# Kernel optimization log

Measured on AMD Instinct MI355X. Metric: run time of the kernel, lower is better.

Reference implementation:

```python
import jax, jax.numpy as jnp
import numpy as np

N_DR, N_P, N_DIS = 8000, 20000, 5000
N_MF, N_BP, N_CC, N_PATH = 3000, 8000, 2000, 2392
H, B = 128, 65536
F_FINGER, F_SEQ, F_DIS = 1024, 400, 512
EPS = 1e-5


def _gcn(e, xs, ndst, W, b):
    # DGL GraphConv(norm='none', in==out): sum-aggregate src feats, then linear, then ReLU
    agg = jax.ops.segment_sum(xs[e[0]], e[1], num_segments=ndst)
    return jax.nn.relu(agg @ W + b)


def _sage(e, xs, xd, Wp, bp, Ws, Wn, b):
    # DGL SAGEConv(aggregator_type='pool'): max over relu(fc_pool(src)) + fc_self(dst), then ReLU
    h = jax.nn.relu(xs @ Wp + bp)
    agg = jax.ops.segment_max(h[e[0]], e[1], num_segments=xd.shape[0])
    agg = jnp.where(jnp.isfinite(agg), agg, 0.0)  # zero-in-degree dst -> 0 (DGL convention)
    return jax.nn.relu(xd @ Ws + agg @ Wn + b)


def _bn_relu(x, g, b):
    # BatchNorm1d in training mode (batch stats, biased var) + ReLU
    m = x.mean(0)
    v = x.var(0)
    return jax.nn.relu(g * (x - m) * jax.lax.rsqrt(v + EPS) + b)


def setup_inputs():
    key = jax.random.key(0)
    ks = iter(jax.random.split(key, 80))
    def nrm(shape, s=0.05):
        return jax.random.normal(next(ks), shape, dtype=jnp.float32) * s
    def edges(E, ns, nd):
        k1, k2 = jax.random.split(next(ks))
        return jnp.stack([jax.random.randint(k1, (E,), 0, ns, dtype=jnp.int32),
                          jax.random.randint(k2, (E,), 0, nd, dtype=jnp.int32)])
    inp = {}
    inp["x_dr"] = jax.random.randint(next(ks), (B, 1), 0, N_DR, dtype=jnp.int32)
    inp["x_p"] = jax.random.randint(next(ks), (B, 1), 0, N_P, dtype=jnp.int32)
    inp["finger_feats"] = nrm((N_DR, F_FINGER), 1.0)
    inp["seq_feats"] = nrm((N_P, F_SEQ), 1.0)
    inp["disease_feat"] = nrm((N_DIS, F_DIS), 1.0)
    inp["MF_feat"] = jnp.eye(N_MF, dtype=jnp.float32)   # identity feats, as in source
    inp["BP_feat"] = jnp.eye(N_BP, dtype=jnp.float32)
    inp["CC_feat"] = jnp.eye(N_CC, dtype=jnp.float32)
    inp["Pathway_feat"] = jnp.eye(N_PATH, dtype=jnp.float32)
    inp["e_dtdr"] = edges(100000, N_DIS, N_DR)
    inp["e_dmdr"] = edges(100000, N_DIS, N_DR)
    inp["e_dp"] = edges(200000, N_DIS, N_P)
    inp["e_drtd"] = edges(100000, N_DR, N_DIS)
    inp["e_drmd"] = edges(100000, N_DR, N_DIS)
    inp["e_pd"] = edges(200000, N_P, N_DIS)
    inp["e_ddi"] = edges(300000, N_DR, N_DR)
    inp["e_ppi"] = edges(600000, N_P, N_P)
    inp["e_mf_sim"] = edges(100000, N_MF, N_MF)
    inp["e_bp_sim"] = edges(300000, N_BP, N_BP)
    inp["e_cc_sim"] = edges(60000, N_CC, N_CC)
    inp["e_mf2p"] = edges(200000, N_MF, N_P)
    inp["e_bp2p"] = edges(400000, N_BP, N_P)
    inp["e_cc2p"] = edges(100000, N_CC, N_P)
    inp["e_path2p"] = edges(100000, N_PATH, N_P)
    inp["W_dr_emb"] = nrm((F_FINGER, H)); inp["b_dr_emb"] = jnp.zeros((H,), jnp.float32)
    inp["W_p_emb"] = nrm((F_SEQ, H)); inp["b_p_emb"] = jnp.zeros((H,), jnp.float32)
    inp["W_d_emb"] = nrm((F_DIS, H)); inp["b_d_emb"] = jnp.zeros((H,), jnp.float32)
    inp["W_mf_emb"] = nrm((N_MF, H)); inp["b_mf_emb"] = jnp.zeros((H,), jnp.float32)
    inp["W_bp_emb"] = nrm((N_BP, H)); inp["b_bp_emb"] = jnp.zeros((H,), jnp.float32)
    inp["W_cc_emb"] = nrm((N_CC, H)); inp["b_cc_emb"] = jnp.zeros((H,), jnp.float32)
    inp["W_path_emb"] = nrm((N_PATH, H)); inp["b_path_emb"] = jnp.zeros((H,), jnp.float32)
    inp["W_gcn"] = nrm((7, H, H)); inp["b_gcn"] = jnp.zeros((7, H), jnp.float32)
    inp["Wp_sage"] = nrm((8, H, H)); inp["bp_sage"] = jnp.zeros((8, H), jnp.float32)
    inp["Ws_sage"] = nrm((8, H, H)); inp["Wn_sage"] = nrm((8, H, H))
    inp["b_sage"] = jnp.zeros((8, H), jnp.float32)
    inp["W1"] = nrm((7 * H, 2 * H)); inp["b1"] = jnp.zeros((2 * H,), jnp.float32)
    inp["g1"] = jnp.ones((2 * H,), jnp.float32); inp["be1"] = jnp.zeros((2 * H,), jnp.float32)
    inp["W2"] = nrm((2 * H, H)); inp["b2"] = jnp.zeros((H,), jnp.float32)
    inp["g2"] = jnp.ones((H,), jnp.float32); inp["be2"] = jnp.zeros((H,), jnp.float32)
    inp["W3"] = nrm((H, 64)); inp["b3"] = jnp.zeros((64,), jnp.float32)
    inp["g3"] = jnp.ones((64,), jnp.float32); inp["be3"] = jnp.zeros((64,), jnp.float32)
    inp["Wo"] = nrm((64, 1)); inp["bo"] = jnp.zeros((1,), jnp.float32)
    return inp


def reference(x_dr, x_p, e_dtdr, e_dmdr, e_dp, e_drtd, e_drmd, e_pd, e_ddi, e_ppi,
              e_mf_sim, e_bp_sim, e_cc_sim, e_mf2p, e_bp2p, e_cc2p, e_path2p,
              finger_feats, seq_feats, disease_feat, MF_feat, BP_feat, CC_feat, Pathway_feat,
              W_dr_emb, b_dr_emb, W_p_emb, b_p_emb, W_d_emb, b_d_emb,
              W_mf_emb, b_mf_emb, W_bp_emb, b_bp_emb, W_cc_emb, b_cc_emb, W_path_emb, b_path_emb,
              W_gcn, b_gcn, Wp_sage, bp_sage, Ws_sage, Wn_sage, b_sage,
              W1, b1, g1, be1, W2, b2, g2, be2, W3, b3, g3, be3, Wo, bo):
    relu = jax.nn.relu
    # node-type input embeddings (Linear + ReLU)
    h_dr0 = relu(finger_feats @ W_dr_emb + b_dr_emb)
    h_p0 = relu(seq_feats @ W_p_emb + b_p_emb)
    h_d = relu(disease_feat @ W_d_emb + b_d_emb)
    h_mf = relu(MF_feat @ W_mf_emb + b_mf_emb)
    h_bp = relu(BP_feat @ W_bp_emb + b_bp_emb)
    h_cc = relu(CC_feat @ W_cc_emb + b_cc_emb)
    h_path = relu(Pathway_feat @ W_path_emb + b_path_emb)
    # GO similarity GCNs with residual
    mf = _gcn(e_mf_sim, h_mf, N_MF, W_gcn[0], b_gcn[0]) + h_mf
    bp = _gcn(e_bp_sim, h_bp, N_BP, W_gcn[1], b_gcn[1]) + h_bp
    cc = _gcn(e_cc_sim, h_cc, N_CC, W_gcn[2], b_gcn[2]) + h_cc
    # GO->protein and pathway->protein (HeteroGraphConv, sum aggregate)
    h_p_go = (_gcn(e_mf2p, mf, N_P, W_gcn[3], b_gcn[3])
              + _gcn(e_bp2p, bp, N_P, W_gcn[4], b_gcn[4])
              + _gcn(e_cc2p, cc, N_P, W_gcn[5], b_gcn[5]))
    h_p_path = _gcn(e_path2p, h_path, N_P, W_gcn[6], b_gcn[6])
    # heterogeneous SAGE layer over my_G (weights shared across the two applications)
    def S(i):
        return (Wp_sage[i], bp_sage[i], Ws_sage[i], Wn_sage[i], b_sage[i])
    def hetero(hdr, hp, hd):
        dr = (_sage(e_dtdr, hd, hdr, *S(0)) + _sage(e_dmdr, hd, hdr, *S(1))
              + _sage(e_ddi, hdr, hdr, *S(6)))
        p = _sage(e_dp, hd, hp, *S(2)) + _sage(e_ppi, hp, hp, *S(7))
        d = (_sage(e_drtd, hdr, hd, *S(3)) + _sage(e_drmd, hdr, hd, *S(4))
             + _sage(e_pd, hp, hd, *S(5)))
        return dr, p, d
    dr1, p1, d1 = hetero(h_dr0, h_p0, h_d)
    dr2, p2, _ = hetero(dr1, p1, d1)
    dr_new = jnp.concatenate([h_dr0, dr1, dr2], axis=1)                 # [N_DR, 3H]
    p_new = jnp.concatenate([h_p0, p1, p2, h_p_go + h_p_path], axis=1)  # [N_P, 4H]
    h = jnp.concatenate([dr_new[x_dr[:, 0]], p_new[x_p[:, 0]]], axis=1)  # [B, 7H]
    h = _bn_relu(h @ W1 + b1, g1, be1)
    h = _bn_relu(h @ W2 + b2, g2, be2)
    h = _bn_relu(h @ W3 + b3, g3, be3)
    return jax.nn.sigmoid(h @ Wo + bo)
```

## Files before the change

kernel.cpp:

```cpp
#include <hip/hip_runtime.h>

#define NCSR 15
#define MAXP 6
#define MAXT 8
#define MAXG 12
#define NPT 21
#define NWT 37

typedef __attribute__((ext_vector_type(8))) short bfrag;
typedef __attribute__((ext_vector_type(4))) float ffrag;

__device__ __forceinline__ float b2f(unsigned short s) {
  return __uint_as_float(((unsigned int)s) << 16);
}
__device__ __forceinline__ unsigned short f2b(float f) {
  unsigned int u = __float_as_uint(f);
  u = (u + 0x7FFFu + ((u >> 16) & 1u)) >> 16;
  return (unsigned short)u;
}
__device__ __forceinline__ float ldf(const void* p, size_t i, int bf) {
  if (bf) return b2f(((const unsigned short*)p)[i]);
  return ((const float*)p)[i];
}
__device__ __forceinline__ int4 ld8(const void* p, size_t i, int bf) {
  if (bf) return *(const int4*)((const unsigned short*)p + i);
  const float* pf = (const float*)p + i;
  float4 f0 = *(const float4*)pf;
  float4 f1 = *(const float4*)(pf + 4);
  int4 v;
  v.x = (int)((unsigned)f2b(f0.x) | ((unsigned)f2b(f0.y) << 16));
  v.y = (int)((unsigned)f2b(f0.z) | ((unsigned)f2b(f0.w) << 16));
  v.z = (int)((unsigned)f2b(f1.x) | ((unsigned)f2b(f1.y) << 16));
  v.w = (int)((unsigned)f2b(f1.z) | ((unsigned)f2b(f1.w) << 16));
  return v;
}

struct CsrDesc {
  const int* src; const int* dst; int E; int n_dst;
  int* rowptr; unsigned short* csrc; int* slot; int pad;
};
struct CsrArgs { CsrDesc d[NCSR]; };

struct PTask { const void* src; float* dst; int n; int pad; };
struct PArgs { PTask t[NPT]; };

struct WTask { const void* src; unsigned short* dst; int K; int N; int eoff; int pad; };
struct WArgs { WTask t[NWT]; };

struct MPass { const unsigned short* A; const unsigned short* W; const float* bias; int lda; int ldw; int flags; };
struct MTask {
  MPass p[MAXP];
  const unsigned short* R; unsigned short* C;
  int npass, n, K, ldc, relu, pad;
};

struct GTask { const int* rowptr; const unsigned short* csrc; const unsigned short* X; unsigned short* out; int n_dst; int ldx; int mode; int pad; };

struct ETask { const void* A; const unsigned short* W; const float* bias; unsigned short* C; int n, K, ldc, pad; };
struct EArgs { ETask t[3]; };

struct BTask { const void* w; const float* b; unsigned short* out; int n; int pad[3]; };
struct BArgs { BTask t[4]; };

struct GSup { GTask t[MAXG]; int off[MAXG + 1]; int nt; };
struct MSup { MTask t[MAXT]; int off[MAXT + 1]; int nt; };

__device__ __forceinline__ int find_task(const int* off, int nt, int bx, int& lx) {
  int t = 0;
  while (t + 1 < nt && bx >= off[t + 1]) ++t;
  lx = bx - off[t];
  return t;
}


__device__ void count_body(const CsrDesc& cd, int lx) {
  for (int e = lx * 256 + (int)threadIdx.x; e < cd.E; e += 96 * 256)
    cd.slot[e] = atomicAdd(&cd.rowptr[cd.dst[e] + 1], 1);
}

__device__ void fill_body(const CsrDesc& cd, int lx) {
  for (int e = lx * 256 + (int)threadIdx.x; e < cd.E; e += 96 * 256) {
    int d = cd.dst[e];
    cd.csrc[cd.rowptr[d] + cd.slot[e]] = (unsigned short)cd.src[e];
  }
}

__device__ void bias_body(const BTask& T, int lx, int bf) {
  const int n8 = T.n >> 3;
  for (int i = lx * 256 + (int)threadIdx.x; i < n8; i += 128 * 256) {
    int base = i << 3;
    int4 v = ld8(T.w, (size_t)base, bf);
    const unsigned short* pv = (const unsigned short*)&v;
    const int cb = base & 127;
    unsigned short o[8];
#pragma unroll
    for (int j = 0; j < 8; ++j) {
      float f = b2f(pv[j]) + T.b[cb + j];
      o[j] = f2b(f > 0.f ? f : 0.f);
    }
    *(int4*)(T.out + base) = *(const int4*)o;
  }
}

__device__ void gather_body(const GTask& T, int lx) {
  int w = lx * 4 + ((int)threadIdx.x >> 6);
  if (w >= T.n_dst) return;
  int lane = threadIdx.x & 63;
  int beg = T.rowptr[w], end = T.rowptr[w + 1];
  float a0 = 0.f, a1 = 0.f;
  int j = beg;
  if (T.mode == 0) {
    for (; j + 3 < end; j += 4) {
      unsigned int u0 = ((const unsigned int*)(T.X + (size_t)T.csrc[j] * T.ldx))[lane];
      unsigned int u1 = ((const unsigned int*)(T.X + (size_t)T.csrc[j + 1] * T.ldx))[lane];
      unsigned int u2 = ((const unsigned int*)(T.X + (size_t)T.csrc[j + 2] * T.ldx))[lane];
      unsigned int u3 = ((const unsigned int*)(T.X + (size_t)T.csrc[j + 3] * T.ldx))[lane];
      a0 += __uint_as_float(u0 << 16) + __uint_as_float(u1 << 16)
          + __uint_as_float(u2 << 16) + __uint_as_float(u3 << 16);
      a1 += __uint_as_float(u0 & 0xFFFF0000u) + __uint_as_float(u1 & 0xFFFF0000u)
          + __uint_as_float(u2 & 0xFFFF0000u) + __uint_as_float(u3 & 0xFFFF0000u);
    }
    for (; j < end; ++j) {
      unsigned int u0 = ((const unsigned int*)(T.X + (size_t)T.csrc[j] * T.ldx))[lane];
      a0 += __uint_as_float(u0 << 16);
      a1 += __uint_as_float(u0 & 0xFFFF0000u);
    }
  } else {
    for (; j + 3 < end; j += 4) {
      unsigned int u0 = ((const unsigned int*)(T.X + (size_t)T.csrc[j] * T.ldx))[lane];
      unsigned int u1 = ((const unsigned int*)(T.X + (size_t)T.csrc[j + 1] * T.ldx))[lane];
      unsigned int u2 = ((const unsigned int*)(T.X + (size_t)T.csrc[j + 2] * T.ldx))[lane];
      unsigned int u3 = ((const unsigned int*)(T.X + (size_t)T.csrc[j + 3] * T.ldx))[lane];
      a0 = fmaxf(fmaxf(a0, fmaxf(__uint_as_float(u0 << 16), __uint_as_float(u1 << 16))),
                 fmaxf(__uint_as_float(u2 << 16), __uint_as_float(u3 << 16)));
      a1 = fmaxf(fmaxf(a1, fmaxf(__uint_as_float(u0 & 0xFFFF0000u), __uint_as_float(u1 & 0xFFFF0000u))),
                 fmaxf(__uint_as_float(u2 & 0xFFFF0000u), __uint_as_float(u3 & 0xFFFF0000u)));
    }
    for (; j < end; ++j) {
      unsigned int u0 = ((const unsigned int*)(T.X + (size_t)T.csrc[j] * T.ldx))[lane];
      a0 = fmaxf(a0, __uint_as_float(u0 << 16));
      a1 = fmaxf(a1, __uint_as_float(u0 & 0xFFFF0000u));
    }
  }
  unsigned int* po = (unsigned int*)(T.out + (size_t)w * 128);
  po[lane] = (unsigned int)f2b(a0) | ((unsigned int)f2b(a1) << 16);
}

__device__ void mg_body(const MTask* T, int lx) {
  const int n = T->n;
  const int row0 = lx * 64;
  if (row0 >= n) return;
  __shared__ __align__(16) unsigned short As[64][72];
  __shared__ __align__(16) unsigned short Ws[128][72];
  const int t = threadIdx.x;
  const int wave = t >> 6, lane = t & 63;
  const int m16 = lane & 15, kq = lane >> 4;
  const int K = T->K;
  ffrag acc[4][2], accO[4][2];
#pragma unroll
  for (int i = 0; i < 4; ++i)
#pragma unroll
    for (int j = 0; j < 2; ++j) { acc[i][j] = (ffrag)0.f; accO[i][j] = (ffrag)0.f; }
  const int colbase = wave * 32;
  for (int ip = 0; ip < T->npass; ++ip) {
    const unsigned short* Ap = T->p[ip].A;
    const unsigned short* Wp = T->p[ip].W;
    const int lda = T->p[ip].lda, ldw = T->p[ip].ldw;
    for (int k0 = 0; k0 < K; k0 += 64) {
      __syncthreads();
#pragma unroll
      for (int e = t; e < 512; e += 256) {
        int r = e >> 3, c = e & 7;
        int row = row0 + r;
        int4 v = {0, 0, 0, 0};
        if (row < n) v = *(const int4*)(Ap + (size_t)row * lda + k0 + c * 8);
        *(int4*)&As[r][c * 8] = v;
      }
#pragma unroll
      for (int e = t; e < 1024; e += 256) {
        int nn = e >> 3, c = e & 7;
        *(int4*)&Ws[nn][c * 8] = *(const int4*)(Wp + (size_t)nn * ldw + k0 + c * 8);
      }
      __syncthreads();
#pragma unroll
      for (int kk = 0; kk < 64; kk += 32) {
        bfrag b0 = *(const bfrag*)&Ws[colbase + m16][kk + kq * 8];
        bfrag b1 = *(const bfrag*)&Ws[colbase + 16 + m16][kk + kq * 8];
#pragma unroll
        for (int rb = 0; rb < 4; ++rb) {
          bfrag a = *(const bfrag*)&As[rb * 16 + m16][kk + kq * 8];
          acc[rb][0] = __builtin_amdgcn_mfma_f32_16x16x32_bf16(a, b0, acc[rb][0], 0, 0, 0);
          acc[rb][1] = __builtin_amdgcn_mfma_f32_16x16x32_bf16(a, b1, acc[rb][1], 0, 0, 0);
        }
      }
    }
    if (T->p[ip].flags & 1) {
      const float* bias = T->p[ip].bias;
      float bv0 = bias ? bias[colbase + m16] : 0.f;
      float bv1 = bias ? bias[colbase + 16 + m16] : 0.f;
#pragma unroll
      for (int rb = 0; rb < 4; ++rb)
#pragma unroll
        for (int cb = 0; cb < 2; ++cb) {
          float bv = cb ? bv1 : bv0;
#pragma unroll
          for (int r = 0; r < 4; ++r) {
            float v = acc[rb][cb][r] + bv;
            if (T->relu) v = v > 0.f ? v : 0.f;
            accO[rb][cb][r] += v;
          }
          acc[rb][cb] = (ffrag)0.f;
        }
    }
  }
  const int ldc = T->ldc;
#pragma unroll
  for (int rb = 0; rb < 4; ++rb)
#pragma unroll
    for (int cb = 0; cb < 2; ++cb) {
      int col = colbase + cb * 16 + m16;
#pragma unroll
      for (int r = 0; r < 4; ++r) {
        int row = row0 + rb * 16 + kq * 4 + r;
        if (row < n) {
          float v = accO[rb][cb][r];
          if (T->R) v += b2f(T->R[(size_t)row * ldc + col]);
          T->C[(size_t)row * ldc + col] = f2b(v);
        }
      }
    }
}

__device__ void embed_body(const ETask& T, int lx, int bf) {
  const int n = T.n;
  const int row0 = lx * 32;
  if (row0 >= n) return;
  __shared__ __align__(16) unsigned short As[32][72];
  __shared__ __align__(16) unsigned short Ws[128][72];
  const int t = threadIdx.x;
  const int wave = t >> 6, lane = t & 63;
  const int m16 = lane & 15, kq = lane >> 4;
  const int K = T.K;
  ffrag acc[2][2];
#pragma unroll
  for (int i = 0; i < 2; ++i)
#pragma unroll
    for (int j = 0; j < 2; ++j) acc[i][j] = (ffrag)0.f;
  const int colbase = wave * 32;
  for (int k0 = 0; k0 < K; k0 += 64) {
    __syncthreads();
    {
      int r = t >> 3, c = t & 7;
      int row = row0 + r, k = k0 + c * 8;
      int4 v = {0, 0, 0, 0};
      if (row < n && k < K) v = ld8(T.A, (size_t)row * K + k, bf);
      *(int4*)&As[r][c * 8] = v;
    }
#pragma unroll
    for (int e = t; e < 1024; e += 256) {
      int nn = e >> 3, c = e & 7;
      int4 v = {0, 0, 0, 0};
      if (k0 + c * 8 < K) v = *(const int4*)(T.W + (size_t)nn * K + k0 + c * 8);
      *(int4*)&Ws[nn][c * 8] = v;
    }
    __syncthreads();
#pragma unroll
    for (int kk = 0; kk < 64; kk += 32) {
      bfrag a0 = *(const bfrag*)&As[m16][kk + kq * 8];
      bfrag a1 = *(const bfrag*)&As[16 + m16][kk + kq * 8];
      bfrag b0 = *(const bfrag*)&Ws[colbase + m16][kk + kq * 8];
      bfrag b1 = *(const bfrag*)&Ws[colbase + 16 + m16][kk + kq * 8];
      acc[0][0] = __builtin_amdgcn_mfma_f32_16x16x32_bf16(a0, b0, acc[0][0], 0, 0, 0);
      acc[0][1] = __builtin_amdgcn_mfma_f32_16x16x32_bf16(a0, b1, acc[0][1], 0, 0, 0);
      acc[1][0] = __builtin_amdgcn_mfma_f32_16x16x32_bf16(a1, b0, acc[1][0], 0, 0, 0);
      acc[1][1] = __builtin_amdgcn_mfma_f32_16x16x32_bf16(a1, b1, acc[1][1], 0, 0, 0);
    }
  }
#pragma unroll
  for (int rb = 0; rb < 2; ++rb)
#pragma unroll
    for (int cb = 0; cb < 2; ++cb) {
      int col = colbase + cb * 16 + m16;
      float bv = T.bias[col];
#pragma unroll
      for (int r = 0; r < 4; ++r) {
        int row = row0 + rb * 16 + kq * 4 + r;
        if (row < n) {
          float v = acc[rb][cb][r] + bv;
          T.C[(size_t)row * T.ldc + col] = f2b(v > 0.f ? v : 0.f);
        }
      }
    }
}


__global__ void k_flag(const unsigned int* probe, int* flag) {
  if (threadIdx.x == 0) *flag = (probe[0] == 0x3F800000u) ? 0 : 1;
}

__launch_bounds__(256)
__global__ void k_cv(PArgs pa, WArgs wa, const int* __restrict__ flagp) {
  const int bf = *flagp;
  int bx = blockIdx.x;
  if (bx < NPT * 4) {
    const PTask T = pa.t[bx >> 2];
    for (int i = (bx & 3) * 256 + (int)threadIdx.x; i < T.n; i += 4 * 256)
      T.dst[i] = ldf(T.src, (size_t)i, bf);
  } else {
    bx -= NPT * 4;
    const WTask T = wa.t[bx >> 5];
    const int lx = bx & 31;
    const int total = T.K * T.N;
    const size_t eoff = (size_t)T.eoff;
    for (int i = lx * 256 + (int)threadIdx.x; i < total; i += 32 * 256) {
      int n = i / T.K, k = i - n * T.K;
      T.dst[i] = f2b(ldf(T.src, eoff + (size_t)k * T.N + n, bf));
    }
  }
}

__launch_bounds__(256)
__global__ void k_prep(CsrArgs csr, EArgs ea, BArgs ba, const int* __restrict__ flagp) {
  int bx = blockIdx.x;
  if (bx < NCSR * 96) { count_body(csr.d[bx / 96], bx % 96); return; }
  bx -= NCSR * 96;
  if (bx < 1032) {
    int t, lx;
    if (bx < 250) { t = 0; lx = bx; }
    else if (bx < 875) { t = 1; lx = bx - 250; }
    else { t = 2; lx = bx - 875; }
    embed_body(ea.t[t], lx, *flagp);
    return;
  }
  bx -= 1032;
  bias_body(ba.t[bx >> 7], bx & 127, *flagp);
}

__global__ void k_csr_scan(CsrArgs args) {
  const CsrDesc cd = args.d[blockIdx.x];
  const int n = cd.n_dst + 1;
  const int t = threadIdx.x;
  const int lane = t & 63, w = t >> 6;
  __shared__ int wsum[16];
  int carry = 0;
  for (int base = 0; base < n; base += 1024) {
    int i = base + t;
    int v = (i < n) ? cd.rowptr[i] : 0;
    for (int off = 1; off < 64; off <<= 1) {
      int u = __shfl_up(v, off, 64);
      if (lane >= off) v += u;
    }
    if (lane == 63) wsum[w] = v;
    __syncthreads();
    if (w == 0) {
      int s = (lane < 16) ? wsum[lane] : 0;
      for (int off = 1; off < 16; off <<= 1) {
        int u = __shfl_up(s, off, 64);
        if (lane >= off) s += u;
      }
      if (lane < 16) wsum[lane] = s;
    }
    __syncthreads();
    int nv = v + carry + (w > 0 ? wsum[w - 1] : 0);
    if (i < n) cd.rowptr[i] = nv;
    carry += wsum[15];
    __syncthreads();
  }
}

__launch_bounds__(256)
__global__ void k_fillmg(CsrArgs csr, MSup ms) {
  int bx = blockIdx.x;
  if (bx < NCSR * 96) { fill_body(csr.d[bx / 96], bx % 96); return; }
  bx -= NCSR * 96;
  int lx; int t = find_task(ms.off, ms.nt, bx, lx);
  mg_body(&ms.t[t], lx);
}

__global__ void k_gsup(GSup gs) {
  int lx; int t = find_task(gs.off, gs.nt, blockIdx.x, lx);
  gather_body(gs.t[t], lx);
}

__launch_bounds__(256)
__global__ void k_gm(GSup gs, MSup ms) {
  int bx = blockIdx.x;
  const int gtot = gs.off[gs.nt];
  if (bx < gtot) {
    int lx; int t = find_task(gs.off, gs.nt, bx, lx);
    gather_body(gs.t[t], lx);
    return;
  }
  bx -= gtot;
  int lx; int t = find_task(ms.off, ms.nt, bx, lx);
  mg_body(&ms.t[t], lx);
}

template<int NC>
__launch_bounds__(256)
__global__ void k_gemm_bn(const unsigned short* __restrict__ A, const unsigned short* __restrict__ W,
                          const float* __restrict__ bias, const float* __restrict__ ss,
                          unsigned short* __restrict__ C, double* __restrict__ st, int n, int K) {
  constexpr int CB = NC / 64;
  __shared__ __align__(16) unsigned short As[64][72];
  __shared__ __align__(16) unsigned short Ws[NC][72];
  const int t = threadIdx.x;
  const int wave = t >> 6, lane = t & 63;
  const int m16 = lane & 15, kq = lane >> 4;
  const int row0 = blockIdx.x * 64;
  if (row0 >= n) return;
  ffrag acc[4][CB];
#pragma unroll
  for (int i = 0; i < 4; ++i)
#pragma unroll
    for (int j = 0; j < CB; ++j) acc[i][j] = (ffrag)0.f;
  const int colbase = wave * 16 * CB;
  for (int k0 = 0; k0 < K; k0 += 64) {
    __syncthreads();
#pragma unroll
    for (int e = t; e < 512; e += 256) {
      int r = e >> 3, c = e & 7;
      int row = row0 + r, k = k0 + c * 8;
      int4 v = {0, 0, 0, 0};
      if (row < n) {
        int4 a8 = *(const int4*)(A + (size_t)row * K + k);
        const unsigned short* pa = (const unsigned short*)&a8;
        unsigned short o[8];
#pragma unroll
        for (int j = 0; j < 8; ++j) {
          float val = fmaf(b2f(pa[j]), ss[k + j], ss[K + k + j]);
          o[j] = f2b(val > 0.f ? val : 0.f);
        }
        v = *(const int4*)o;
      }
      *(int4*)&As[r][c * 8] = v;
    }
#pragma unroll
    for (int e = t; e < NC * 8; e += 256) {
      int nn = e >> 3, c = e & 7;
      *(int4*)&Ws[nn][c * 8] = *(const int4*)(W + (size_t)nn * K + k0 + c * 8);
    }
    __syncthreads();
#pragma unroll
    for (int kk = 0; kk < 64; kk += 32) {
#pragma unroll
      for (int cb = 0; cb < CB; ++cb) {
        bfrag b = *(const bfrag*)&Ws[colbase + cb * 16 + m16][kk + kq * 8];
#pragma unroll
        for (int rb = 0; rb < 4; ++rb) {
          bfrag a = *(const bfrag*)&As[rb * 16 + m16][kk + kq * 8];
          acc[rb][cb] = __builtin_amdgcn_mfma_f32_16x16x32_bf16(a, b, acc[rb][cb], 0, 0, 0);
        }
      }
    }
  }
#pragma unroll
  for (int cb = 0; cb < CB; ++cb) {
    int col = colbase + cb * 16 + m16;
    float bv = bias[col];
    float cs = 0.f, cq = 0.f;
#pragma unroll
    for (int rb = 0; rb < 4; ++rb) {
#pragma unroll
      for (int r = 0; r < 4; ++r) {
        int row = row0 + rb * 16 + kq * 4 + r;
        if (row < n) {
          float v = acc[rb][cb][r] + bv;
          C[(size_t)row * NC + col] = f2b(v);
          cs += v; cq += v * v;
        }
      }
    }
    cs += __shfl_xor(cs, 16); cs += __shfl_xor(cs, 32);
    cq += __shfl_xor(cq, 16); cq += __shfl_xor(cq, 32);
    if (kq == 0) {
      atomicAdd(&st[col], (double)cs);
      atomicAdd(&st[NC + col], (double)cq);
    }
  }
}

__global__ void k_hstat(const int* __restrict__ xdr, const int* __restrict__ xp,
                        const unsigned short* __restrict__ Udr, const unsigned short* __restrict__ Up,
                        double* __restrict__ st, int B) {
  __shared__ double sS[4][256];
  __shared__ double sQ[4][256];
  const int t = threadIdx.x;
  const int lane = t & 63, w = t >> 6;
  const int c4 = lane * 4;
  double s0 = 0, s1 = 0, s2 = 0, s3 = 0, q0 = 0, q1 = 0, q2 = 0, q3 = 0;
  const int NW = gridDim.x * 4;
  for (int r = blockIdx.x * 4 + w; r < B; r += NW) {
    int i = xdr[r], j = xp[r];
    uint2 a = *(const uint2*)(Udr + (size_t)i * 256 + c4);
    uint2 b = *(const uint2*)(Up + (size_t)j * 256 + c4);
    float v0 = b2f((unsigned short)a.x) + b2f((unsigned short)b.x);
    float v1 = b2f((unsigned short)(a.x >> 16)) + b2f((unsigned short)(b.x >> 16));
    float v2 = b2f((unsigned short)a.y) + b2f((unsigned short)b.y);
    float v3 = b2f((unsigned short)(a.y >> 16)) + b2f((unsigned short)(b.y >> 16));
    s0 += v0; s1 += v1; s2 += v2; s3 += v3;
    q0 += (double)v0 * (double)v0; q1 += (double)v1 * (double)v1;
    q2 += (double)v2 * (double)v2; q3 += (double)v3 * (double)v3;
  }
  sS[w][c4] = s0; sS[w][c4 + 1] = s1; sS[w][c4 + 2] = s2; sS[w][c4 + 3] = s3;
  sQ[w][c4] = q0; sQ[w][c4 + 1] = q1; sQ[w][c4 + 2] = q2; sQ[w][c4 + 3] = q3;
  __syncthreads();
  double ts = sS[0][t] + sS[1][t] + sS[2][t] + sS[3][t];
  double tq = sQ[0][t] + sQ[1][t] + sQ[2][t] + sQ[3][t];
  atomicAdd(&st[t], ts);
  atomicAdd(&st[256 + t], tq);
}

__launch_bounds__(256)
__global__ void k_gemm_bn1(const int* __restrict__ xdr, const int* __restrict__ xp,
                           const unsigned short* __restrict__ Udr, const unsigned short* __restrict__ Up,
                           const unsigned short* __restrict__ W, const float* __restrict__ bias,
                           const float* __restrict__ ss, unsigned short* __restrict__ Co,
                           double* __restrict__ st, int n) {
  __shared__ __align__(16) unsigned short As[64][72];
  __shared__ __align__(16) unsigned short Ws[128][72];
  __shared__ int gi[64], gj[64];
  const int t = threadIdx.x;
  const int wave = t >> 6, lane = t & 63;
  const int m16 = lane & 15, kq = lane >> 4;
  const int row0 = blockIdx.x * 64;
  if (row0 >= n) return;
  if (t < 64) {
    int row = row0 + t; if (row >= n) row = n - 1;
    gi[t] = xdr[row]; gj[t] = xp[row];
  }
  ffrag acc[4][2];
#pragma unroll
  for (int i = 0; i < 4; ++i)
#pragma unroll
    for (int j = 0; j < 2; ++j) acc[i][j] = (ffrag)0.f;
  const int colbase = wave * 32;
  __syncthreads();
  for (int k0 = 0; k0 < 256; k0 += 64) {
    __syncthreads();
#pragma unroll
    for (int e = t; e < 512; e += 256) {
      int r = e >> 3, seg = e & 7;
      int k = k0 + seg * 8;
      int4 a = *(const int4*)(Udr + (size_t)gi[r] * 256 + k);
      int4 b = *(const int4*)(Up + (size_t)gj[r] * 256 + k);
      const unsigned short* pa = (const unsigned short*)&a;
      const unsigned short* pb = (const unsigned short*)&b;
      unsigned short o[8];
#pragma unroll
      for (int jj = 0; jj < 8; ++jj) {
        float v = b2f(pa[jj]) + b2f(pb[jj]);
        v = fmaf(v, ss[k + jj], ss[256 + k + jj]);
        o[jj] = f2b(v > 0.f ? v : 0.f);
      }
      *(int4*)&As[r][seg * 8] = *(const int4*)o;
    }
#pragma unroll
    for (int e = t; e < 1024; e += 256) {
      int nn = e >> 3, c = e & 7;
      *(int4*)&Ws[nn][c * 8] = *(const int4*)(W + (size_t)nn * 256 + k0 + c * 8);
    }
    __syncthreads();
#pragma unroll
    for (int kk = 0; kk < 64; kk += 32) {
      bfrag b0 = *(const bfrag*)&Ws[colbase + m16][kk + kq * 8];
      bfrag b1 = *(const bfrag*)&Ws[colbase + 16 + m16][kk + kq * 8];
#pragma unroll
      for (int rb = 0; rb < 4; ++rb) {
        bfrag a = *(const bfrag*)&As[rb * 16 + m16][kk + kq * 8];
        acc[rb][0] = __builtin_amdgcn_mfma_f32_16x16x32_bf16(a, b0, acc[rb][0], 0, 0, 0);
        acc[rb][1] = __builtin_amdgcn_mfma_f32_16x16x32_bf16(a, b1, acc[rb][1], 0, 0, 0);
      }
    }
  }
#pragma unroll
  for (int cb = 0; cb < 2; ++cb) {
    int col = colbase + cb * 16 + m16;
    float bv = bias[col];
    float cs = 0.f, cq = 0.f;
#pragma unroll
    for (int rb = 0; rb < 4; ++rb) {
#pragma unroll
      for (int r = 0; r < 4; ++r) {
        int row = row0 + rb * 16 + kq * 4 + r;
        if (row < n) {
          float v = acc[rb][cb][r] + bv;
          Co[(size_t)row * 128 + col] = f2b(v);
          cs += v; cq += v * v;
        }
      }
    }
    cs += __shfl_xor(cs, 16); cs += __shfl_xor(cs, 32);
    cq += __shfl_xor(cq, 16); cq += __shfl_xor(cq, 32);
    if (kq == 0) {
      atomicAdd(&st[col], (double)cs);
      atomicAdd(&st[128 + col], (double)cq);
    }
  }
}

__global__ void k_bnfin(const double* __restrict__ st, int B, int C,
                        const float* __restrict__ g, const float* __restrict__ be,
                        float* __restrict__ ss) {
  int c = threadIdx.x;
  if (c < C) {
    double m = st[c] / B;
    double v = st[C + c] / B - m * m;
    if (v < 0) v = 0;
    float sc = (float)((double)g[c] / sqrt(v + 1e-5));
    ss[c] = sc;
    ss[C + c] = be[c] - (float)m * sc;
  }
}

__global__ void k_final(const unsigned short* __restrict__ Z3, const float* __restrict__ ss3,
                        const float* __restrict__ Wo, const float* __restrict__ bo,
                        void* __restrict__ out, int B, const int* __restrict__ flagp) {
  __shared__ float w[64], sc[64], sh[64];
  if (threadIdx.x < 64) {
    w[threadIdx.x] = Wo[threadIdx.x];
    sc[threadIdx.x] = ss3[threadIdx.x];
    sh[threadIdx.x] = ss3[64 + threadIdx.x];
  }
  __syncthreads();
  const int bf = *flagp;
  const float bb = bo[0];
  for (int r = blockIdx.x * blockDim.x + threadIdx.x; r < B; r += gridDim.x * blockDim.x) {
    const unsigned short* z = &Z3[(size_t)r * 64];
    float acc = bb;
#pragma unroll
    for (int k = 0; k < 64; ++k) {
      float y = fmaf(b2f(z[k]), sc[k], sh[k]);
      y = y > 0.f ? y : 0.f;
      acc = fmaf(y, w[k], acc);
    }
    float sv = 1.f / (1.f + expf(-acc));
    if (bf) ((unsigned short*)out)[r] = f2b(sv);
    else ((float*)out)[r] = sv;
  }
}

extern "C" void kernel_launch(void* const* d_in, const int* in_sizes, int n_in,
                              void* d_out, int out_size, void* d_ws, size_t ws_size,
                              hipStream_t stream) {
  enum { N_DR = 8000, N_P = 20000, N_DIS = 5000, N_MF = 3000, N_BP = 8000,
         N_CC = 2000, N_PATH = 2392 };
  if (n_in < 59) return;
  const int B = in_sizes[0];
  const int* x_dr = (const int*)d_in[0];
  const int* x_p  = (const int*)d_in[1];

  char* base = (char*)d_ws;
  size_t off = 0;
  auto alloc = [&](size_t bytes) -> void* {
    void* p = base + off;
    off += (bytes + 255) & ~(size_t)255;
    return p;
  };
  int*    flagp = (int*)alloc(256);
  double* st1 = (double*)alloc(896 * sizeof(double));
  double* st2 = st1 + 512; double* st3 = st2 + 256;
  float*  ss1 = (float*)alloc(896 * sizeof(float));
  float*  ss2 = ss1 + 512; float* ss3 = ss2 + 256;
  float*  pbuf = (float*)alloc(6000 * sizeof(float));
  unsigned short* wbf = (unsigned short*)alloc(1100000 * 2);
  unsigned short* DR  = (unsigned short*)alloc((size_t)N_DR * 384 * 2);
  unsigned short* P   = (unsigned short*)alloc((size_t)N_P * 512 * 2);
  unsigned short* h_d = (unsigned short*)alloc((size_t)N_DIS * 128 * 2);
  unsigned short* d1b = (unsigned short*)alloc((size_t)N_DIS * 128 * 2);
  unsigned short* z1  = (unsigned short*)alloc((size_t)B * 256 * 2);
  char* arena = (char*)alloc(44u * 1024 * 1024);
  if (off > ws_size) return;

  unsigned short* ar = (unsigned short*)arena;
  unsigned short* A_hmf  = ar;
  unsigned short* A_hbp  = A_hmf + (size_t)N_MF * 128;
  unsigned short* A_hcc  = A_hbp + (size_t)N_BP * 128;
  unsigned short* A_hpath= A_hcc + (size_t)N_CC * 128;
  unsigned short* A_gomf = A_hpath + (size_t)N_PATH * 128;
  unsigned short* A_gobp = A_gomf + (size_t)N_MF * 128;
  unsigned short* A_gocc = A_gobp + (size_t)N_BP * 128;
  unsigned short* ag17 = A_gocc + (size_t)N_CC * 128;
  unsigned short* ag18 = ag17 + (size_t)N_MF * 128;
  unsigned short* ag9  = ag18 + (size_t)N_BP * 128;
  unsigned short* ag10 = ag9  + (size_t)N_DR * 128;
  unsigned short* ag11 = ag10 + (size_t)N_DR * 128;
  unsigned short* ag12 = ag11 + (size_t)N_P * 128;
  unsigned short* ag13 = ag12 + (size_t)N_DIS * 128;
  unsigned short* ag14 = ag13 + (size_t)N_DIS * 128;
  unsigned short* ag15 = ag14 + (size_t)N_DIS * 128;
  unsigned short* ag16 = ag15 + (size_t)N_DR * 128;
  unsigned short* ag21 = ag16 + (size_t)N_P * 128;
  unsigned short* ag22 = ag21 + (size_t)N_P * 128;
  unsigned short* ag23 = ag22 + (size_t)N_P * 128;
  unsigned short* U_dr = ar;
  unsigned short* U_p  = U_dr + (size_t)N_DR * 256;
  unsigned short* z2 = U_p + (size_t)N_P * 256;
  unsigned short* z3 = z1;
  int* slot_arena = (int*)(ar + (size_t)7168000);

  k_flag<<<1, 64, 0, stream>>>((const unsigned int*)d_in[5], flagp);

  float* pp[59] = {};
  PArgs pa;
  {
    const int pidx[NPT] = {25,27,29,31,33,35,37,39,41,44,46,47,48,50,51,52,54,55,56,57,58};
    size_t poff = 0;
    for (int l = 0; l < NPT; ++l) {
      int i = pidx[l];
      pa.t[l].src = d_in[i]; pa.t[l].dst = pbuf + poff; pa.t[l].n = in_sizes[i]; pa.t[l].pad = 0;
      pp[i] = pbuf + poff;
      poff += in_sizes[i];
    }
  }
  unsigned short *Wdr_t, *Wpe_t, *Wde_t, *Wg_t, *Wps_t, *Wss_t, *Wns_t, *W1_t, *W2_t, *W3_t;
  WArgs wa;
  {
    int l = 0; size_t woff = 0;
    auto add = [&](int inIdx, int eoff, int K, int N) -> unsigned short* {
      unsigned short* dst = wbf + woff;
      wa.t[l].src = d_in[inIdx]; wa.t[l].dst = dst; wa.t[l].K = K; wa.t[l].N = N;
      wa.t[l].eoff = eoff; wa.t[l].pad = 0;
      ++l; woff += (size_t)K * N;
      return dst;
    };
    Wdr_t = add(24, 0, 1024, 128);
    Wpe_t = add(26, 0, 400, 128);
    Wde_t = add(28, 0, 512, 128);
    Wg_t = wbf + woff;
    for (int j = 0; j < 7; ++j) add(38, j * 16384, 128, 128);
    Wps_t = wbf + woff;
    for (int j = 0; j < 8; ++j) add(40, j * 16384, 128, 128);
    Wss_t = wbf + woff;
    for (int j = 0; j < 8; ++j) add(42, j * 16384, 128, 128);
    Wns_t = wbf + woff;
    for (int j = 0; j < 8; ++j) add(43, j * 16384, 128, 128);
    W1_t = add(45, 0, 896, 256);
    W2_t = add(49, 0, 256, 128);
    W3_t = add(53, 0, 128, 64);
  }
  k_cv<<<NPT * 4 + NWT * 32, 256, 0, stream>>>(pa, wa, flagp);

  const int list_ei[NCSR] = {9, 10, 11, 12, 13, 14, 15, 16, 17, 18, 19, 20, 21, 22, 23};
  const int list_nd[NCSR] = {N_DR, N_DR, N_P, N_DIS, N_DIS, N_DIS, N_DR, N_P,
                             N_MF, N_BP, N_CC, N_P, N_P, N_P, N_P};
  int* rp[24]; unsigned short* cs[24];
  CsrArgs csra;
  unsigned short* csr_end;
  {
    int* ip = (int*)z1;
    int* rp0 = ip;
    for (int l = 0; l < NCSR; ++l) { csra.d[l].rowptr = ip; rp[list_ei[l]] = ip; ip += list_nd[l] + 1; }
    size_t rp_total = (size_t)(ip - rp0);
    unsigned short* up = (unsigned short*)ip;
    size_t slotoff = 0;
    for (int l = 0; l < NCSR; ++l) {
      int ei = list_ei[l];
      int E = in_sizes[ei] / 2;
      csra.d[l].src = (const int*)d_in[ei];
      csra.d[l].dst = (const int*)d_in[ei] + E;
      csra.d[l].E = E;
      csra.d[l].n_dst = list_nd[l];
      csra.d[l].csrc = up; cs[ei] = up;
      csra.d[l].slot = slot_arena + slotoff;
      csra.d[l].pad = 0;
      up += E;
      slotoff += E;
    }
    csr_end = up;
    hipMemsetAsync(rp0, 0, rp_total * sizeof(int), stream);
  }
  unsigned short* plb = (unsigned short*)(((uintptr_t)csr_end + 255) & ~(uintptr_t)255);
  unsigned short* plz0 = plb;
  unsigned short* plz1 = plz0 + (size_t)N_DIS * 128;
  unsigned short* plz2 = plz1 + (size_t)N_DIS * 128;
  unsigned short* plz3 = plz2 + (size_t)N_DIS * 128;
  unsigned short* plz4 = plz3 + (size_t)N_DR * 128;
  unsigned short* plz5 = plz4 + (size_t)N_DR * 128;
  unsigned short* plz6 = plz5 + (size_t)N_P * 128;
  unsigned short* plz7 = plz6 + (size_t)N_DR * 128;
  unsigned short* ag19 = plz7 + (size_t)N_P * 128;
  unsigned short* ag20 = ag19 + (size_t)N_CC * 128;
  if ((ag20 + (size_t)N_P * 128) > (z1 + (size_t)B * 256)) return;

  hipMemsetAsync(st1, 0, 896 * sizeof(double), stream);

  auto mkpass = [](MTask& T, int i, const unsigned short* A, int lda, const unsigned short* W,
                   int ldw, const float* bias, int end) {
    T.p[i].A = A; T.p[i].lda = lda; T.p[i].W = W; T.p[i].ldw = ldw;
    T.p[i].bias = bias; T.p[i].flags = end;
  };
  const float* bg = pp[39];
  const float* bp_s = pp[41];
  const float* b_s = pp[44];

  auto gadd = [](GSup& g, GTask t) {
    if (g.nt == 0) g.off[0] = 0;
    g.t[g.nt] = t;
    g.off[g.nt + 1] = g.off[g.nt] + (t.n_dst + 3) / 4;
    g.nt++;
  };
  auto madd = [](MSup& m, const MTask& t) {
    if (m.nt == 0) m.off[0] = 0;
    m.t[m.nt] = t;
    m.off[m.nt + 1] = m.off[m.nt] + (t.n + 63) / 64;
    m.nt++;
  };

  {
    EArgs ea;
    ea.t[0] = {d_in[2], Wdr_t, pp[25], DR, N_DR, 1024, 384, 0};
    ea.t[1] = {d_in[3], Wpe_t, pp[27], P, N_P, 400, 512, 0};
    ea.t[2] = {d_in[4], Wde_t, pp[29], h_d, N_DIS, 512, 128, 0};
    BArgs ba;
    ba.t[0] = {d_in[30], pp[31], A_hmf, N_MF * 128, {}};
    ba.t[1] = {d_in[32], pp[33], A_hbp, N_BP * 128, {}};
    ba.t[2] = {d_in[34], pp[35], A_hcc, N_CC * 128, {}};
    ba.t[3] = {d_in[36], pp[37], A_hpath, N_PATH * 128, {}};
    k_prep<<<NCSR * 96 + 1032 + 4 * 128, 256, 0, stream>>>(csra, ea, ba, flagp);
  }

  k_csr_scan<<<NCSR, 1024, 0, stream>>>(csra);

  {
    MSup ms; ms.nt = 0;
    const unsigned short* xs[8] = {h_d, h_d, h_d, DR, DR, P, DR, P};
    const int lda[8] = {128, 128, 128, 384, 384, 512, 384, 512};
    const int nn[8] = {N_DIS, N_DIS, N_DIS, N_DR, N_DR, N_P, N_DR, N_P};
    unsigned short* plo[8] = {plz0, plz1, plz2, plz3, plz4, plz5, plz6, plz7};
    for (int i = 0; i < 8; ++i) {
      MTask T;
      mkpass(T, 0, xs[i], lda[i], Wps_t + (size_t)i * 16384, 128, bp_s + i * 128, 1);
      T.npass = 1; T.n = nn[i]; T.K = 128; T.R = nullptr; T.C = plo[i]; T.ldc = 128; T.relu = 1;
      madd(ms, T);
    }
    k_fillmg<<<NCSR * 96 + ms.off[ms.nt], 256, 0, stream>>>(csra, ms);
  }

  {
    GSup gs; gs.nt = 0;
    gadd(gs, {rp[17], cs[17], A_hmf, ag17, N_MF, 128, 0, 0});
    gadd(gs, {rp[18], cs[18], A_hbp, ag18, N_BP, 128, 0, 0});
    gadd(gs, {rp[19], cs[19], A_hcc, ag19, N_CC, 128, 0, 0});
    gadd(gs, {rp[9],  cs[9],  plz0, ag9,  N_DR, 128, 1, 0});
    gadd(gs, {rp[10], cs[10], plz1, ag10, N_DR, 128, 1, 0});
    gadd(gs, {rp[11], cs[11], plz2, ag11, N_P, 128, 1, 0});
    gadd(gs, {rp[12], cs[12], plz3, ag12, N_DIS, 128, 1, 0});
    gadd(gs, {rp[13], cs[13], plz4, ag13, N_DIS, 128, 1, 0});
    gadd(gs, {rp[14], cs[14], plz5, ag14, N_DIS, 128, 1, 0});
    gadd(gs, {rp[15], cs[15], plz6, ag15, N_DR, 128, 1, 0});
    gadd(gs, {rp[16], cs[16], plz7, ag16, N_P, 128, 1, 0});
    k_gsup<<<gs.off[gs.nt], 256, 0, stream>>>(gs);
  }

  GSup g0; g0.nt = 0; g0.off[0] = 0;

  {
    MSup ms; ms.nt = 0;
    for (int i = 0; i < 3; ++i) {
      MTask T;
      const unsigned short* aggp = (i == 0) ? ag17 : (i == 1) ? ag18 : ag19;
      const unsigned short* Rp = (i == 0) ? A_hmf : (i == 1) ? A_hbp : A_hcc;
      unsigned short* Cp = (i == 0) ? A_gomf : (i == 1) ? A_gobp : A_gocc;
      int n = (i == 0) ? N_MF : (i == 1) ? N_BP : N_CC;
      mkpass(T, 0, aggp, 128, Wg_t + (size_t)i * 16384, 128, bg + i * 128, 1);
      T.npass = 1; T.n = n; T.K = 128; T.R = Rp; T.C = Cp; T.ldc = 128; T.relu = 1;
      madd(ms, T);
    }
    {
      MTask T;
      mkpass(T, 0, DR, 384, Wss_t + (size_t)0 * 16384, 128, nullptr, 0);
      mkpass(T, 1, ag9, 128, Wns_t + (size_t)0 * 16384, 128, b_s + 0 * 128, 1);
      mkpass(T, 2, DR, 384, Wss_t + (size_t)1 * 16384, 128, nullptr, 0);
      mkpass(T, 3, ag10, 128, Wns_t + (size_t)1 * 16384, 128, b_s + 1 * 128, 1);
      mkpass(T, 4, DR, 384, Wss_t + (size_t)6 * 16384, 128, nullptr, 0);
      mkpass(T, 5, ag15, 128, Wns_t + (size_t)6 * 16384, 128, b_s + 6 * 128, 1);
      T.npass = 6; T.n = N_DR; T.K = 128; T.R = nullptr; T.C = DR + 128; T.ldc = 384; T.relu = 1;
      madd(ms, T);
    }
    {
      MTask T;
      mkpass(T, 0, P, 512, Wss_t + (size_t)2 * 16384, 128, nullptr, 0);
      mkpass(T, 1, ag11, 128, Wns_t + (size_t)2 * 16384, 128, b_s + 2 * 128, 1);
      mkpass(T, 2, P, 512, Wss_t + (size_t)7 * 16384, 128, nullptr, 0);
      mkpass(T, 3, ag16, 128, Wns_t + (size_t)7 * 16384, 128, b_s + 7 * 128, 1);
      T.npass = 4; T.n = N_P; T.K = 128; T.R = nullptr; T.C = P + 128; T.ldc = 512; T.relu = 1;
      madd(ms, T);
    }
    {
      MTask T;
      mkpass(T, 0, h_d, 128, Wss_t + (size_t)3 * 16384, 128, nullptr, 0);
      mkpass(T, 1, ag12, 128, Wns_t + (size_t)3 * 16384, 128, b_s + 3 * 128, 1);
      mkpass(T, 2, h_d, 128, Wss_t + (size_t)4 * 16384, 128, nullptr, 0);
      mkpass(T, 3, ag13, 128, Wns_t + (size_t)4 * 16384, 128, b_s + 4 * 128, 1);
      mkpass(T, 4, h_d, 128, Wss_t + (size_t)5 * 16384, 128, nullptr, 0);
      mkpass(T, 5, ag14, 128, Wns_t + (size_t)5 * 16384, 128, b_s + 5 * 128, 1);
      T.npass = 6; T.n = N_DIS; T.K = 128; T.R = nullptr; T.C = d1b; T.ldc = 128; T.relu = 1;
      madd(ms, T);
    }
    k_gm<<<ms.off[ms.nt], 256, 0, stream>>>(g0, ms);
  }

  {
    GSup gs; gs.nt = 0;
    gadd(gs, {rp[20], cs[20], A_gomf, ag20, N_P, 128, 0, 0});
    gadd(gs, {rp[21], cs[21], A_gobp, ag21, N_P, 128, 0, 0});
    gadd(gs, {rp[22], cs[22], A_gocc, ag22, N_P, 128, 0, 0});
    gadd(gs, {rp[23], cs[23], A_hpath, ag23, N_P, 128, 0, 0});
    MSup ms; ms.nt = 0;
    const unsigned short* xs[5] = {d1b, d1b, d1b, DR + 128, P + 128};
    const int lda[5] = {128, 128, 128, 384, 512};
    const int nn[5] = {N_DIS, N_DIS, N_DIS, N_DR, N_P};
    unsigned short* plo[5] = {plz0, plz1, plz2, plz6, plz7};
    const int si[5] = {0, 1, 2, 6, 7};
    for (int i = 0; i < 5; ++i) {
      MTask T;
      mkpass(T, 0, xs[i], lda[i], Wps_t + (size_t)si[i] * 16384, 128, bp_s + si[i] * 128, 1);
      T.npass = 1; T.n = nn[i]; T.K = 128; T.R = nullptr; T.C = plo[i]; T.ldc = 128; T.relu = 1;
      madd(ms, T);
    }
    k_gm<<<gs.off[gs.nt] + ms.off[ms.nt], 256, 0, stream>>>(gs, ms);
  }

  {
    GSup gs; gs.nt = 0;
    gadd(gs, {rp[9],  cs[9],  plz0, ag9,  N_DR, 128, 1, 0});
    gadd(gs, {rp[10], cs[10], plz1, ag10, N_DR, 128, 1, 0});
    gadd(gs, {rp[11], cs[11], plz2, ag11, N_P, 128, 1, 0});
    gadd(gs, {rp[15], cs[15], plz6, ag15, N_DR, 128, 1, 0});
    gadd(gs, {rp[16], cs[16], plz7, ag16, N_P, 128, 1, 0});
    MSup ms; ms.nt = 0;
    MTask T;
    mkpass(T, 0, ag20, 128, Wg_t + 3 * 16384, 128, bg + 3 * 128, 1);
    mkpass(T, 1, ag21, 128, Wg_t + 4 * 16384, 128, bg + 4 * 128, 1);
    mkpass(T, 2, ag22, 128, Wg_t + 5 * 16384, 128, bg + 5 * 128, 1);
    mkpass(T, 3, ag23, 128, Wg_t + 6 * 16384, 128, bg + 6 * 128, 1);
    T.npass = 4; T.n = N_P; T.K = 128; T.R = nullptr; T.C = P + 384; T.ldc = 512; T.relu = 1;
    madd(ms, T);
    k_gm<<<gs.off[gs.nt] + ms.off[ms.nt], 256, 0, stream>>>(gs, ms);
  }

  {
    MSup ms; ms.nt = 0;
    {
      MTask T;
      mkpass(T, 0, DR + 128, 384, Wss_t + (size_t)0 * 16384, 128, nullptr, 0);
      mkpass(T, 1, ag9, 128, Wns_t + (size_t)0 * 16384, 128, b_s + 0 * 128, 1);
      mkpass(T, 2, DR + 128, 384, Wss_t + (size_t)1 * 16384, 128, nullptr, 0);
      mkpass(T, 3, ag10, 128, Wns_t + (size_t)1 * 16384, 128, b_s + 1 * 128, 1);
      mkpass(T, 4, DR + 128, 384, Wss_t + (size_t)6 * 16384, 128, nullptr, 0);
      mkpass(T, 5, ag15, 128, Wns_t + (size_t)6 * 16384, 128, b_s + 6 * 128, 1);
      T.npass = 6; T.n = N_DR; T.K = 128; T.R = nullptr; T.C = DR + 256; T.ldc = 384; T.relu = 1;
      madd(ms, T);
    }
    {
      MTask T;
      mkpass(T, 0, P + 128, 512, Wss_t + (size_t)2 * 16384, 128, nullptr, 0);
      mkpass(T, 1, ag11, 128, Wns_t + (size_t)2 * 16384, 128, b_s + 2 * 128, 1);
      mkpass(T, 2, P + 128, 512, Wss_t + (size_t)7 * 16384, 128, nullptr, 0);
      mkpass(T, 3, ag16, 128, Wns_t + (size_t)7 * 16384, 128, b_s + 7 * 128, 1);
      T.npass = 4; T.n = N_P; T.K = 128; T.R = nullptr; T.C = P + 256; T.ldc = 512; T.relu = 1;
      madd(ms, T);
    }
    k_gm<<<ms.off[ms.nt], 256, 0, stream>>>(g0, ms);
  }

  {
    MSup ms; ms.nt = 0;
    for (int half = 0; half < 2; ++half) {
      {
        MTask T;
        mkpass(T, 0, DR, 384, W1_t + (size_t)(half * 128) * 896, 896, pp[46] + half * 128, 1);
        T.npass = 1; T.n = N_DR; T.K = 384; T.R = nullptr;
        T.C = U_dr + half * 128; T.ldc = 256; T.relu = 0;
        madd(ms, T);
      }
      {
        MTask T;
        mkpass(T, 0, P, 512, W1_t + (size_t)(half * 128) * 896 + 384, 896, nullptr, 1);
        T.npass = 1; T.n = N_P; T.K = 512; T.R = nullptr;
        T.C = U_p + half * 128; T.ldc = 256; T.relu = 0;
        madd(ms, T);
      }
    }
    k_gm<<<ms.off[ms.nt], 256, 0, stream>>>(g0, ms);
  }

  k_hstat<<<256, 256, 0, stream>>>(x_dr, x_p, U_dr, U_p, st1, B);
  k_bnfin<<<1, 256, 0, stream>>>(st1, B, 256, pp[47], pp[48], ss1);

  k_gemm_bn1<<<(B + 63) / 64, 256, 0, stream>>>(x_dr, x_p, U_dr, U_p, W2_t, pp[50], ss1, z2, st2, B);
  k_bnfin<<<1, 128, 0, stream>>>(st2, B, 128, pp[51], pp[52], ss2);

  k_gemm_bn<64><<<(B + 63) / 64, 256, 0, stream>>>(z2, W3_t, pp[54], ss2, z3, st3, B, 128);
  k_bnfin<<<1, 64, 0, stream>>>(st3, B, 64, pp[55], pp[56], ss3);

  k_final<<<256, 256, 0, stream>>>(z3, ss3, pp[57], pp[58], d_out, B, flagp);
}
```

Before: 1.282 ms.

## Build CSR counts with per-chunk LDS histograms instead of global atomics

Replaces the global atomicAdd degree counting with a kernel where each block takes a 16K-edge chunk and builds a packed 16-bit histogram in shared memory, writing per-chunk counts and 16-bit local slots. The scan kernel first does a per-destination exclusive scan over chunks to produce chunk offsets and degrees, and the fill step combines rowptr, chunk offset and local slot. This removes contended global atomics and the rowptr memset, and halves slot storage, at the cost of an extra count array and a serial per-destination loop over chunks in the single-block-per-graph scan kernel.

Result: slower. 1.389 ms (+8.4%).

```diff
diff --git a/kernel.cpp b/kernel.cpp
--- a/kernel.cpp
+++ b/kernel.cpp
@@ -6,6 +6,8 @@
 #define MAXG 12
 #define NPT 21
 #define NWT 37
+#define CLOG 14
+#define CCHUNK 16384
 
 typedef __attribute__((ext_vector_type(8))) short bfrag;
 typedef __attribute__((ext_vector_type(4))) float ffrag;
@@ -36,10 +38,13 @@
 }
 
 struct CsrDesc {
-  const int* src; const int* dst; int E; int n_dst;
-  int* rowptr; unsigned short* csrc; int* slot; int pad;
+  const int* src; const int* dst; int* rowptr; unsigned short* csrc;
+  unsigned short* slot16;
+  unsigned int* cnt;
+  int E, n_dst, nb, pad;
 };
 struct CsrArgs { CsrDesc d[NCSR]; };
+struct COff { int off[16]; };
 
 struct PTask { const void* src; float* dst; int n; int pad; };
 struct PArgs { PTask t[NPT]; };
@@ -73,15 +78,12 @@
 }
 
 
-__device__ void count_body(const CsrDesc& cd, int lx) {
-  for (int e = lx * 256 + (int)threadIdx.x; e < cd.E; e += 96 * 256)
-    cd.slot[e] = atomicAdd(&cd.rowptr[cd.dst[e] + 1], 1);
-}
-
 __device__ void fill_body(const CsrDesc& cd, int lx) {
   for (int e = lx * 256 + (int)threadIdx.x; e < cd.E; e += 96 * 256) {
     int d = cd.dst[e];
-    cd.csrc[cd.rowptr[d] + cd.slot[e]] = (unsigned short)cd.src[e];
+    int pos = cd.rowptr[d] + (int)cd.cnt[(size_t)(e >> CLOG) * cd.n_dst + d]
+              + (int)cd.slot16[e];
+    cd.csrc[pos] = (unsigned short)cd.src[e];
   }
 }
 
@@ -299,6 +301,44 @@
 }
 
 __launch_bounds__(256)
+__global__ void k_csr_cnt(CsrArgs args, COff co) {
+  __shared__ unsigned int h32[10000];
+  int bx = blockIdx.x, l = 0;
+  while (l + 1 < NCSR && bx >= co.off[l + 1]) ++l;
+  const int b = bx - co.off[l];
+  const CsrDesc cd = args.d[l];
+  const int nh = (cd.n_dst + 1) >> 1;
+  for (int i = threadIdx.x; i < nh; i += 256) h32[i] = 0;
+  __syncthreads();
+  const int e0 = b << CLOG;
+  const int e1 = min(e0 + CCHUNK, cd.E);
+  for (int e = e0 + (int)threadIdx.x; e < e1; e += 256) {
+    int d = cd.dst[e];
+    unsigned int old = atomicAdd(&h32[d >> 1], (d & 1) ? 65536u : 1u);
+    cd.slot16[e] = (unsigned short)((d & 1) ? (old >> 16) : (old & 0xFFFFu));
+  }
+  __syncthreads();
+  unsigned int* cb = cd.cnt + (size_t)b * cd.n_dst;
+  for (int i = threadIdx.x; i < cd.n_dst; i += 256)
+    cb[i] = (i & 1) ? (h32[i >> 1] >> 16) : (h32[i >> 1] & 0xFFFFu);
+}
+
+__launch_bounds__(256)
+__global__ void k_eb(EArgs ea, BArgs ba, const int* __restrict__ flagp) {
+  int bx = blockIdx.x;
+  if (bx < 1032) {
+    int t, lx;
+    if (bx < 250) { t = 0; lx = bx; }
+    else if (bx < 875) { t = 1; lx = bx - 250; }
+    else { t = 2; lx = bx - 875; }
+    embed_body(ea.t[t], lx, *flagp);
+    return;
+  }
+  bx -= 1032;
+  bias_body(ba.t[bx >> 7], bx & 127, *flagp);
+}
+
+__launch_bounds__(256)
 __global__ void k_cv(PArgs pa, WArgs wa, const int* __restrict__ flagp) {
   const int bf = *flagp;
   int bx = blockIdx.x;
@@ -319,27 +359,23 @@
   }
 }
 
-__launch_bounds__(256)
-__global__ void k_prep(CsrArgs csr, EArgs ea, BArgs ba, const int* __restrict__ flagp) {
-  int bx = blockIdx.x;
-  if (bx < NCSR * 96) { count_body(csr.d[bx / 96], bx % 96); return; }
-  bx -= NCSR * 96;
-  if (bx < 1032) {
-    int t, lx;
-    if (bx < 250) { t = 0; lx = bx; }
-    else if (bx < 875) { t = 1; lx = bx - 250; }
-    else { t = 2; lx = bx - 875; }
-    embed_body(ea.t[t], lx, *flagp);
-    return;
-  }
-  bx -= 1032;
-  bias_body(ba.t[bx >> 7], bx & 127, *flagp);
-}
-
 __global__ void k_csr_scan(CsrArgs args) {
   const CsrDesc cd = args.d[blockIdx.x];
+  const int t = threadIdx.x;
+  const int nb = cd.nb;
+  for (int d = t; d < cd.n_dst; d += 1024) {
+    unsigned int s = 0;
+    unsigned int* cc = cd.cnt + d;
+    for (int b = 0; b < nb; ++b) {
+      unsigned int v = cc[(size_t)b * cd.n_dst];
+      cc[(size_t)b * cd.n_dst] = s;
+      s += v;
+    }
+    cd.rowptr[d + 1] = (int)s;
+  }
+  if (t == 0) cd.rowptr[0] = 0;
+  __syncthreads();
   const int n = cd.n_dst + 1;
-  const int t = threadIdx.x;
   const int lane = t & 63, w = t >> 6;
   __shared__ int wsum[16];
   int carry = 0;
@@ -669,7 +705,7 @@
   unsigned short* h_d = (unsigned short*)alloc((size_t)N_DIS * 128 * 2);
   unsigned short* d1b = (unsigned short*)alloc((size_t)N_DIS * 128 * 2);
   unsigned short* z1  = (unsigned short*)alloc((size_t)B * 256 * 2);
-  char* arena = (char*)alloc(44u * 1024 * 1024);
+  char* arena = (char*)alloc(46u * 1024 * 1024);
   if (off > ws_size) return;
 
   unsigned short* ar = (unsigned short*)arena;
@@ -697,7 +733,43 @@
   unsigned short* U_p  = U_dr + (size_t)N_DR * 256;
   unsigned short* z2 = U_p + (size_t)N_P * 256;
   unsigned short* z3 = z1;
-  int* slot_arena = (int*)(ar + (size_t)7168000);
+  unsigned short* slot_base = ar + (size_t)7168000;
+
+  const int list_ei[NCSR] = {9, 10, 11, 12, 13, 14, 15, 16, 17, 18, 19, 20, 21, 22, 23};
+  const int list_nd[NCSR] = {N_DR, N_DR, N_P, N_DIS, N_DIS, N_DIS, N_DR, N_P,
+                             N_MF, N_BP, N_CC, N_P, N_P, N_P, N_P};
+  int* rp[24]; unsigned short* cs[24];
+  CsrArgs csra;
+  COff coff;
+  unsigned short* csr_end;
+  {
+    int* ip = (int*)z1;
+    for (int l = 0; l < NCSR; ++l) { csra.d[l].rowptr = ip; rp[list_ei[l]] = ip; ip += list_nd[l] + 1; }
+    unsigned short* up = (unsigned short*)ip;
+    unsigned short* sp = slot_base;
+    for (int l = 0; l < NCSR; ++l) {
+      int ei = list_ei[l];
+      int E = in_sizes[ei] / 2;
+      csra.d[l].src = (const int*)d_in[ei];
+      csra.d[l].dst = (const int*)d_in[ei] + E;
+      csra.d[l].E = E;
+      csra.d[l].n_dst = list_nd[l];
+      csra.d[l].nb = (E + CCHUNK - 1) >> CLOG;
+      csra.d[l].csrc = up; cs[ei] = up;
+      csra.d[l].slot16 = sp;
+      up += E;
+      sp += E;
+    }
+    csr_end = up;
+    unsigned int* cp = (unsigned int*)(((uintptr_t)sp + 255) & ~(uintptr_t)255);
+    coff.off[0] = 0;
+    for (int l = 0; l < NCSR; ++l) {
+      csra.d[l].cnt = cp;
+      cp += (size_t)csra.d[l].nb * csra.d[l].n_dst;
+      coff.off[l + 1] = coff.off[l] + csra.d[l].nb;
+    }
+  }
+  k_csr_cnt<<<coff.off[NCSR], 256, 0, stream>>>(csra, coff);
 
   k_flag<<<1, 64, 0, stream>>>((const unsigned int*)d_in[5], flagp);
 
@@ -741,35 +813,6 @@
   }
   k_cv<<<NPT * 4 + NWT * 32, 256, 0, stream>>>(pa, wa, flagp);
 
-  const int list_ei[NCSR] = {9, 10, 11, 12, 13, 14, 15, 16, 17, 18, 19, 20, 21, 22, 23};
-  const int list_nd[NCSR] = {N_DR, N_DR, N_P, N_DIS, N_DIS, N_DIS, N_DR, N_P,
-                             N_MF, N_BP, N_CC, N_P, N_P, N_P, N_P};
-  int* rp[24]; unsigned short* cs[24];
-  CsrArgs csra;
-  unsigned short* csr_end;
-  {
-    int* ip = (int*)z1;
-    int* rp0 = ip;
-    for (int l = 0; l < NCSR; ++l) { csra.d[l].rowptr = ip; rp[list_ei[l]] = ip; ip += list_nd[l] + 1; }
-    size_t rp_total = (size_t)(ip - rp0);
-    unsigned short* up = (unsigned short*)ip;
-    size_t slotoff = 0;
-    for (int l = 0; l < NCSR; ++l) {
-      int ei = list_ei[l];
-      int E = in_sizes[ei] / 2;
-      csra.d[l].src = (const int*)d_in[ei];
-      csra.d[l].dst = (const int*)d_in[ei] + E;
-      csra.d[l].E = E;
-      csra.d[l].n_dst = list_nd[l];
-      csra.d[l].csrc = up; cs[ei] = up;
-      csra.d[l].slot = slot_arena + slotoff;
-      csra.d[l].pad = 0;
-      up += E;
-      slotoff += E;
-    }
-    csr_end = up;
-    hipMemsetAsync(rp0, 0, rp_total * sizeof(int), stream);
-  }
   unsigned short* plb = (unsigned short*)(((uintptr_t)csr_end + 255) & ~(uintptr_t)255);
   unsigned short* plz0 = plb;
   unsigned short* plz1 = plz0 + (size_t)N_DIS * 128;
@@ -817,7 +860,7 @@
     ba.t[1] = {d_in[32], pp[33], A_hbp, N_BP * 128, {}};
     ba.t[2] = {d_in[34], pp[35], A_hcc, N_CC * 128, {}};
     ba.t[3] = {d_in[36], pp[37], A_hpath, N_PATH * 128, {}};
-    k_prep<<<NCSR * 96 + 1032 + 4 * 128, 256, 0, stream>>>(csra, ea, ba, flagp);
+    k_eb<<<1032 + 4 * 128, 256, 0, stream>>>(ea, ba, flagp);
   }
 
   k_csr_scan<<<NCSR, 1024, 0, stream>>>(csra);
```
